# Performance work log

Hardware: AMD Instinct MI355X
Metric: run time of the kernel (lower is better)

The kernel has to match this reference:

```python
import jax, jax.numpy as jnp
import numpy as np

H = 16
D_MODEL = 1024
D_K = D_MODEL // H
WINDOW = 50
ROPE_BASE = 10000.0


def _rope_tables(seq_len, dim, dtype):
    inv_freq = 1.0 / (ROPE_BASE ** (jnp.arange(0, dim, 2, dtype=jnp.float32) / dim))
    t = jnp.arange(seq_len, dtype=jnp.float32)
    freqs = t[:, None] * inv_freq[None, :]          # [S, dim/2]
    emb = jnp.concatenate([freqs, freqs], axis=-1)  # [S, dim]
    return jnp.cos(emb).astype(dtype), jnp.sin(emb).astype(dtype)


def _rotate_half(x):
    d = x.shape[-1] // 2
    return jnp.concatenate([-x[..., d:], x[..., :d]], axis=-1)


def setup_inputs() -> dict:
    key = jax.random.key(0)
    ks = jax.random.split(key, 11)
    B, S = 2, 2048
    scale = 1.0 / np.sqrt(D_MODEL)
    inp = {
        'query': jax.random.normal(ks[0], (B, S, D_MODEL), jnp.float32),
        'key':   jax.random.normal(ks[1], (B, S, D_MODEL), jnp.float32),
        'value': jax.random.normal(ks[2], (B, S, D_MODEL), jnp.float32),
        'Wq': jax.random.normal(ks[3], (D_MODEL, D_MODEL), jnp.float32) * scale,
        'bq': jnp.zeros((D_MODEL,), jnp.float32),
        'Wk': jax.random.normal(ks[4], (D_MODEL, D_MODEL), jnp.float32) * scale,
        'bk': jnp.zeros((D_MODEL,), jnp.float32),
        'Wv': jax.random.normal(ks[5], (D_MODEL, D_MODEL), jnp.float32) * scale,
        'bv': jnp.zeros((D_MODEL,), jnp.float32),
        'Wo': jax.random.normal(ks[6], (D_MODEL, D_MODEL), jnp.float32) * scale,
        'bo': jnp.zeros((D_MODEL,), jnp.float32),
    }
    return inp


def reference(query, key, value, Wq, bq, Wk, bk, Wv, bv, Wo, bo):
    B, S, _ = query.shape
    # QKV projections (torch Linear: x @ W.T + b), split into heads -> [B,H,S,Dk]
    def proj(x, W, b):
        return (x @ W.T + b).reshape(B, S, H, D_K).transpose(0, 2, 1, 3)
    q = proj(query, Wq, bq)
    k = proj(key, Wk, bk)
    v = proj(value, Wv, bv)

    cos, sin = _rope_tables(S, D_K, q.dtype)  # [S, Dk]
    q = q * cos + _rotate_half(q) * sin
    k = k * cos + _rotate_half(k) * sin

    scores = jnp.einsum('bhqd,bhkd->bhqk', q, k) / np.sqrt(D_K)
    # sliding-window mask: |i-j| <= WINDOW
    idx = jnp.arange(S)
    dist = jnp.abs(idx[None, :] - idx[:, None])  # [S, S]
    scores = jnp.where(dist <= WINDOW, scores, jnp.asarray(-1e9, scores.dtype))

    p = jax.nn.softmax(scores, axis=-1)
    out = jnp.einsum('bhqk,bhkd->bhqd', p, v)          # [B,H,S,Dk]
    out = out.transpose(0, 2, 1, 3).reshape(B, S, D_MODEL)
    return out @ Wo.T + bo
```

## Files before the change

### kernel.cpp

```cpp
#include <hip/hip_runtime.h>
#include <hip/hip_bf16.h>
#include <math.h>

typedef __bf16 bf16_t;
typedef __bf16 bf16x8 __attribute__((ext_vector_type(8)));
typedef float floatx4 __attribute__((ext_vector_type(4)));
typedef unsigned int u32;
typedef unsigned short u16;

#define NHEAD 16

__device__ __forceinline__ void gload_lds16(const void* g, void* l) {
    __builtin_amdgcn_global_load_lds((const __attribute__((address_space(1))) u32*)g,
                                     (__attribute__((address_space(3))) u32*)l, 16, 0, 0);
}

__global__ __launch_bounds__(256) void k_prep(
    const float* __restrict__ q, const float* __restrict__ k, const float* __restrict__ v,
    const float* __restrict__ wq, const float* __restrict__ wk,
    const float* __restrict__ wv, const float* __restrict__ wo,
    bf16_t* __restrict__ Xq, bf16_t* __restrict__ Xk, bf16_t* __restrict__ Xv,
    bf16_t* __restrict__ Wqb, bf16_t* __restrict__ Wkb, bf16_t* __restrict__ Wvb,
    bf16_t* __restrict__ Wob, float* __restrict__ ct, float* __restrict__ st)
{
    int b = blockIdx.x;
    if (b < 8192) {
        const float* src; bf16_t* dst; int off;
        if      (b < 2048) { src = q;  dst = Xq;  off = b; }
        else if (b < 4096) { src = k;  dst = Xk;  off = b - 2048; }
        else if (b < 6144) { src = v;  dst = Xv;  off = b - 4096; }
        else if (b < 6656) { src = wq; dst = Wqb; off = b - 6144; }
        else if (b < 7168) { src = wk; dst = Wkb; off = b - 6656; }
        else if (b < 7680) { src = wv; dst = Wvb; off = b - 7168; }
        else               { src = wo; dst = Wob; off = b - 7680; }
        int i = (off * 256 + threadIdx.x) * 8;
        float4 a = *(const float4*)(src + i);
        float4 c = *(const float4*)(src + i + 4);
        bf16x8 o;
        o[0]=(bf16_t)a.x; o[1]=(bf16_t)a.y; o[2]=(bf16_t)a.z; o[3]=(bf16_t)a.w;
        o[4]=(bf16_t)c.x; o[5]=(bf16_t)c.y; o[6]=(bf16_t)c.z; o[7]=(bf16_t)c.w;
        *(bf16x8*)(dst + i) = o;
    } else {
        int idx = (b - 8192) * 256 + threadIdx.x;
        int s = idx >> 5, i = idx & 31;
        float e = (float)(2 * i) / 64.0f;
        float invf = 1.0f / powf(10000.0f, e);
        float ang = (float)s * invf;
        ct[idx] = cosf(ang);
        st[idx] = sinf(ang);
    }
}

__global__ __launch_bounds__(256,3) void k_gemm_qkv(
    const bf16_t* __restrict__ Xq, const bf16_t* __restrict__ Xk, const bf16_t* __restrict__ Xv,
    const bf16_t* __restrict__ Wqb, const bf16_t* __restrict__ Wkb, const bf16_t* __restrict__ Wvb,
    const float* __restrict__ bq, const float* __restrict__ bk, const float* __restrict__ bv,
    bf16_t* __restrict__ Qr, bf16_t* __restrict__ Kr, bf16_t* __restrict__ Vh,
    const float* __restrict__ ct, const float* __restrict__ st)
{
    __shared__ __align__(16) bf16_t As[2][4096];
    __shared__ __align__(16) bf16_t Bs[2][4096];

    int b0 = blockIdx.x;
    int wg = (b0 & 7) * 96 + (b0 >> 3);
    int id  = wg >> 8;
    int bid = wg & 255;

    const bf16_t* A   = (id==0) ? Xq  : (id==1) ? Xk  : Xv;
    const bf16_t* Wt  = (id==0) ? Wqb : (id==1) ? Wkb : Wvb;
    const float*  bias= (id==0) ? bq  : (id==1) ? bk  : bv;
    bf16_t* out = (id==0) ? Qr : (id==1) ? Kr : Vh;
    bool do_rope = (id < 2);

    int bm = (bid >> 3) << 7;
    int bn = (bid & 7) << 7;
    int tid = threadIdx.x;
    int l = tid & 63, wid = tid >> 6;
    int wr = wid >> 1, wc = wid & 1;
    int fr = l & 15, kg = l >> 4;

    floatx4 acc[4][4];
    #pragma unroll
    for (int i = 0; i < 4; ++i)
        #pragma unroll
        for (int j = 0; j < 4; ++j) acc[i][j] = (floatx4){0.f,0.f,0.f,0.f};

    int srow = tid >> 2;
    int scol = ((tid & 3) ^ (srow & 3)) << 3;
    const bf16_t* Ap0 = A  + ((size_t)(bm + srow) << 10) + scol;
    const bf16_t* Ap1 = A  + ((size_t)(bm + 64 + srow) << 10) + scol;
    const bf16_t* Bp0 = Wt + ((size_t)(bn + srow) << 10) + scol;
    const bf16_t* Bp1 = Wt + ((size_t)(bn + 64 + srow) << 10) + scol;

    gload_lds16(Ap0, &As[0][tid << 3]);
    gload_lds16(Ap1, &As[0][(tid + 256) << 3]);
    gload_lds16(Bp0, &Bs[0][tid << 3]);
    gload_lds16(Bp1, &Bs[0][(tid + 256) << 3]);
    __syncthreads();

    int a_off = fr * 64 + ((kg ^ (fr & 3)) << 4);
    int cur = 0;
    for (int t = 0; t < 32; ++t) {
        if (t < 31) {
            int k0 = (t + 1) << 5;
            gload_lds16(Ap0 + k0, &As[cur ^ 1][tid << 3]);
            gload_lds16(Ap1 + k0, &As[cur ^ 1][(tid + 256) << 3]);
            gload_lds16(Bp0 + k0, &Bs[cur ^ 1][tid << 3]);
            gload_lds16(Bp1 + k0, &Bs[cur ^ 1][(tid + 256) << 3]);
        }
        bf16x8 af[4], bfr[4];
        #pragma unroll
        for (int i = 0; i < 4; ++i)
            af[i]  = *(const bf16x8*)((const char*)As[cur] + (((wr << 2) + i) << 10) + a_off);
        #pragma unroll
        for (int j = 0; j < 4; ++j)
            bfr[j] = *(const bf16x8*)((const char*)Bs[cur] + (((wc << 2) + j) << 10) + a_off);
        #pragma unroll
        for (int i = 0; i < 4; ++i)
            #pragma unroll
            for (int j = 0; j < 4; ++j)
                acc[i][j] = __builtin_amdgcn_mfma_f32_16x16x32_bf16(af[i], bfr[j], acc[i][j], 0, 0, 0);
        __syncthreads();
        cur ^= 1;
    }

    int h = (bn + (wc<<6)) >> 6;
    #pragma unroll
    for (int i = 0; i < 4; ++i) {
        #pragma unroll
        for (int r = 0; r < 4; ++r) {
            int m  = bm + (wr<<6) + (i<<4) + (kg<<2) + r;
            int b_ = m >> 11, s_ = m & 2047;
            size_t ob = ((((size_t)(b_*NHEAD + h)) << 11) + s_) << 6;
            if (do_rope) {
                #pragma unroll
                for (int j = 0; j < 2; ++j) {
                    int d = (j<<4) + fr;
                    float lo = acc[i][j][r]   + bias[bn + (wc<<6) + d];
                    float hv = acc[i][j+2][r] + bias[bn + (wc<<6) + d + 32];
                    float c = ct[(s_<<5) + d], sn = st[(s_<<5) + d];
                    out[ob + d]      = (bf16_t)(lo*c - hv*sn);
                    out[ob + d + 32] = (bf16_t)(hv*c + lo*sn);
                }
            } else {
                #pragma unroll
                for (int j = 0; j < 4; ++j) {
                    int d = (j<<4) + fr;
                    out[ob + d] = (bf16_t)(acc[i][j][r] + bias[bn + (wc<<6) + d]);
                }
            }
        }
    }
}

__global__ __launch_bounds__(256,4) void k_gemm_o(
    const bf16_t* __restrict__ A, const bf16_t* __restrict__ Wt,
    const float* __restrict__ bias, float* __restrict__ out)
{
    __shared__ __align__(16) bf16_t As[2][2048];
    __shared__ __align__(16) bf16_t Bs[2][2048];

    int b0 = blockIdx.x;
    int wg = (b0 & 7) * 128 + (b0 >> 3);
    int bm = (wg >> 4) << 6;
    int bn = (wg & 15) << 6;
    int tid = threadIdx.x;
    int l = tid & 63, wid = tid >> 6;
    int fr = l & 15, kg = l >> 4;

    floatx4 acc[4];
    #pragma unroll
    for (int j = 0; j < 4; ++j) acc[j] = (floatx4){0.f,0.f,0.f,0.f};

    int srow = tid >> 2;
    int scol = ((tid & 3) ^ (srow & 3)) << 3;
    const bf16_t* Ap = A  + ((size_t)(bm + srow) << 10) + scol;
    const bf16_t* Bp = Wt + ((size_t)(bn + srow) << 10) + scol;

    gload_lds16(Ap, &As[0][tid << 3]);
    gload_lds16(Bp, &Bs[0][tid << 3]);
    __syncthreads();

    int a_off = fr * 64 + ((kg ^ (fr & 3)) << 4);
    int cur = 0;
    for (int t = 0; t < 32; ++t) {
        if (t < 31) {
            int k0 = (t + 1) << 5;
            gload_lds16(Ap + k0, &As[cur ^ 1][tid << 3]);
            gload_lds16(Bp + k0, &Bs[cur ^ 1][tid << 3]);
        }
        bf16x8 af, bfr[4];
        af = *(const bf16x8*)((const char*)As[cur] + (wid << 10) + a_off);
        #pragma unroll
        for (int j = 0; j < 4; ++j)
            bfr[j] = *(const bf16x8*)((const char*)Bs[cur] + (j << 10) + a_off);
        #pragma unroll
        for (int j = 0; j < 4; ++j)
            acc[j] = __builtin_amdgcn_mfma_f32_16x16x32_bf16(af, bfr[j], acc[j], 0, 0, 0);
        __syncthreads();
        cur ^= 1;
    }

    #pragma unroll
    for (int r = 0; r < 4; ++r) {
        int m = bm + (wid << 4) + (kg << 2) + r;
        #pragma unroll
        for (int j = 0; j < 4; ++j) {
            int n = bn + (j << 4) + fr;
            out[((size_t)m << 10) + n] = acc[j][r] + bias[n];
        }
    }
}

__global__ __launch_bounds__(256,3) void k_attn(
    const bf16_t* __restrict__ Qr, const bf16_t* __restrict__ Kr,
    const bf16_t* __restrict__ Vh, bf16_t* __restrict__ AO)
{
    __shared__ char smem[51200];
    char* KsPs = smem;
    char* VtB  = smem + 25600;

    int q0 = blockIdx.x << 6;
    int h = blockIdx.y, b_ = blockIdx.z;
    int kstart = q0 - 64; if (kstart < 0) kstart = 0;
    int kend   = q0 + 128; if (kend > 2048) kend = 2048;
    int NR = kend - kstart;

    int tid = threadIdx.x, l = tid & 63, w = tid >> 6;
    int lane16 = l & 15, hi8 = (l >> 4) << 3;

    const bf16_t* Kbase = Kr + (((((size_t)(b_*NHEAD + h)) << 11) + kstart) << 6);
    const bf16_t* Vbase = Vh + (((((size_t)(b_*NHEAD + h)) << 11) + kstart) << 6);

    #pragma unroll
    for (int it = 0; it < 6; ++it) {
        int c = tid + (it << 8);
        int y = c << 4;
        int row = y >> 7, oz = y & 127;
        int srw = row < NR ? row : NR - 1;
        int src = (srw << 7) + (oz ^ ((row & 7) << 4));
        gload_lds16((const char*)Kbase + src, KsPs + y);
    }
    #pragma unroll
    for (int it = 0; it < 6; ++it) {
        int c = tid + (it << 8);
        int jd2 = c >> 4;
        int dq  = (c & 15) << 2;
        int j0 = jd2 << 1, j1 = j0 + 1;
        int j0c = j0 < NR ? j0 : NR - 1;
        int j1c = j1 < NR ? j1 : NR - 1;
        ushort4 v0 = *(const ushort4*)(Vbase + (j0c << 6) + dq);
        ushort4 v1 = *(const ushort4*)(Vbase + (j1c << 6) + dq);
        u16 a0[4] = {(u16)v0.x,(u16)v0.y,(u16)v0.z,(u16)v0.w};
        u16 a1[4] = {(u16)v1.x,(u16)v1.y,(u16)v1.z,(u16)v1.w};
        #pragma unroll
        for (int t = 0; t < 4; ++t) {
            int d = dq + t;
            u32 pair = (u32)a0[t] | ((u32)a1[t] << 16);
            *(u32*)(VtB + d * 400 + ((jd2 << 2) ^ (((d >> 3) & 7) << 4))) = pair;
        }
    }
    int qs = q0 + (w << 4) + lane16;
    const bf16_t* Qbase = Qr + (((((size_t)(b_*NHEAD + h)) << 11) + qs) << 6);
    bf16x8 qf0 = *(const bf16x8*)(Qbase + hi8);
    bf16x8 qf1 = *(const bf16x8*)(Qbase + 32 + hi8);

    __syncthreads();

    floatx4 sc[12];
    #pragma unroll
    for (int kt = 0; kt < 12; ++kt) {
        int row = (kt << 4) + lane16;
        int base = (row << 7) + (hi8 << 1);
        int swz = (row & 7) << 4;
        bf16x8 kf0 = *(const bf16x8*)(KsPs + (base ^ swz));
        bf16x8 kf1 = *(const bf16x8*)(KsPs + ((base + 64) ^ swz));
        floatx4 a = (floatx4){0.f,0.f,0.f,0.f};
        a = __builtin_amdgcn_mfma_f32_16x16x32_bf16(qf0, kf0, a, 0, 0, 0);
        a = __builtin_amdgcn_mfma_f32_16x16x32_bf16(qf1, kf1, a, 0, 0, 0);
        sc[kt] = a;
    }

    float inv_[4];
    #pragma unroll
    for (int r = 0; r < 4; ++r) {
        int qrow = q0 + (w << 4) + ((l >> 4) << 2) + r;
        float mx = -1e30f;
        #pragma unroll
        for (int kt = 0; kt < 12; ++kt) {
            int ks = kstart + (kt << 4) + lane16;
            int dd = qrow - ks; dd = dd < 0 ? -dd : dd;
            float sv = sc[kt][r] * 0.125f;
            sv = (dd <= 50 && ks < kend) ? sv : -1e30f;
            sc[kt][r] = sv;
            mx = fmaxf(mx, sv);
        }
        #pragma unroll
        for (int off = 1; off < 16; off <<= 1) mx = fmaxf(mx, __shfl_xor(mx, off));
        float sum = 0.f;
        #pragma unroll
        for (int kt = 0; kt < 12; ++kt) {
            float p = __expf(sc[kt][r] - mx);
            sc[kt][r] = p;
            sum += p;
        }
        #pragma unroll
        for (int off = 1; off < 16; off <<= 1) sum += __shfl_xor(sum, off);
        inv_[r] = 1.0f / sum;
    }

    __syncthreads();

    char* PwB = KsPs + w * 6400;
    #pragma unroll
    for (int r = 0; r < 4; ++r) {
        int prow = ((l >> 4) << 2) + r;
        int pm = ((prow >> 2) & 3) << 4;
        #pragma unroll
        for (int kt = 0; kt < 12; ++kt) {
            int keyoff = ((kt << 4) + lane16) << 1;
            *(bf16_t*)(PwB + prow * 400 + (keyoff ^ pm)) = (bf16_t)(sc[kt][r] * inv_[r]);
        }
    }

    floatx4 oc[4];
    #pragma unroll
    for (int dt = 0; dt < 4; ++dt) oc[dt] = (floatx4){0.f,0.f,0.f,0.f};
    int pm_r = ((lane16 >> 2) & 3) << 4;
    #pragma unroll
    for (int ks = 0; ks < 6; ++ks) {
        int keyoff = ((ks << 5) + hi8) << 1;
        bf16x8 pf = *(const bf16x8*)(PwB + lane16 * 400 + (keyoff ^ pm_r));
        #pragma unroll
        for (int dt = 0; dt < 4; ++dt) {
            int d = (dt << 4) + lane16;
            bf16x8 vf = *(const bf16x8*)(VtB + d * 400 + (keyoff ^ (((d >> 3) & 7) << 4)));
            oc[dt] = __builtin_amdgcn_mfma_f32_16x16x32_bf16(pf, vf, oc[dt], 0, 0, 0);
        }
    }
    #pragma unroll
    for (int dt = 0; dt < 4; ++dt)
        #pragma unroll
        for (int r = 0; r < 4; ++r) {
            int qq = q0 + (w << 4) + ((l >> 4) << 2) + r;
            AO[(((size_t)(b_ * 2048 + qq)) << 10) + (h << 6) + (dt << 4) + lane16] = (bf16_t)oc[dt][r];
        }
}

extern "C" void kernel_launch(void* const* d_in, const int* in_sizes, int n_in,
                              void* d_out, int out_size, void* d_ws, size_t ws_size,
                              hipStream_t stream)
{
    const float* query = (const float*)d_in[0];
    const float* key_  = (const float*)d_in[1];
    const float* value = (const float*)d_in[2];
    const float* Wq = (const float*)d_in[3];
    const float* bq = (const float*)d_in[4];
    const float* Wk = (const float*)d_in[5];
    const float* bk = (const float*)d_in[6];
    const float* Wv = (const float*)d_in[7];
    const float* bv = (const float*)d_in[8];
    const float* Wo = (const float*)d_in[9];
    const float* bo = (const float*)d_in[10];

    char* ws = (char*)d_ws;
    bf16_t* Xq  = (bf16_t*)(ws);
    bf16_t* Xk  = (bf16_t*)(ws + 8388608);
    bf16_t* Xv  = (bf16_t*)(ws + 16777216);
    bf16_t* Wqb = (bf16_t*)(ws + 25165824);
    bf16_t* Wkb = (bf16_t*)(ws + 27262976);
    bf16_t* Wvb = (bf16_t*)(ws + 29360128);
    bf16_t* Wob = (bf16_t*)(ws + 31457280);
    bf16_t* Qr  = (bf16_t*)(ws + 33554432);
    bf16_t* Kr  = (bf16_t*)(ws + 41943040);
    bf16_t* Vh  = (bf16_t*)(ws + 50331648);
    bf16_t* AO  = (bf16_t*)(ws + 58720256);
    float*  ct  = (float*)(ws + 67108864);
    float*  st  = (float*)(ws + 67371008);

    k_prep<<<8448, 256, 0, stream>>>(query, key_, value, Wq, Wk, Wv, Wo,
                                     Xq, Xk, Xv, Wqb, Wkb, Wvb, Wob, ct, st);
    k_gemm_qkv<<<768, 256, 0, stream>>>(Xq, Xk, Xv, Wqb, Wkb, Wvb,
                                        bq, bk, bv, Qr, Kr, Vh, ct, st);
    k_attn<<<dim3(32, 16, 2), 256, 0, stream>>>(Qr, Kr, Vh, AO);
    k_gemm_o<<<1024, 256, 0, stream>>>(AO, Wob, bo, (float*)d_out);
}
```

Before: 94.12 us.

## Transpose attention MFMA operands, read K from global, vectorize P and output stores

The sliding-window attention kernel now reads K fragments straight from global memory instead of staging them in LDS, and swaps the MFMA operand order so each lane owns one query row. That makes the softmax reductions two cross-group shuffles instead of four-step reductions per row. P is written to LDS as packed 64-bit chunks, and the output is staged through LDS so global stores are coalesced 16-byte writes. It also adds s_setprio around the MFMA loops. The risk is uncoalesced, repeated global K reads that replace the shared LDS copy.

```diff
diff --git a/kernel.cpp b/kernel.cpp
--- a/kernel.cpp
+++ b/kernel.cpp
@@ -7,12 +7,18 @@
 typedef float floatx4 __attribute__((ext_vector_type(4)));
 typedef unsigned int u32;
 typedef unsigned short u16;
+typedef unsigned long long u64;
 
 #define NHEAD 16
 
 __device__ __forceinline__ void gload_lds16(const void* g, void* l) {
     __builtin_amdgcn_global_load_lds((const __attribute__((address_space(1))) u32*)g,
                                      (__attribute__((address_space(3))) u32*)l, 16, 0, 0);
+}
+
+__device__ __forceinline__ u32 pack2(float x, float y) {
+    bf16_t a = (bf16_t)x, b = (bf16_t)y;
+    return (u32)*(u16*)&a | ((u32)*(u16*)&b << 16);
 }
 
 __global__ __launch_bounds__(256) void k_prep(
@@ -217,8 +223,8 @@
     const bf16_t* __restrict__ Vh, bf16_t* __restrict__ AO)
 {
     __shared__ char smem[51200];
-    char* KsPs = smem;
-    char* VtB  = smem + 25600;
+    char* VtB  = smem;
+    char* Pall = smem + 25600;
 
     int q0 = blockIdx.x << 6;
     int h = blockIdx.y, b_ = blockIdx.z;
@@ -227,20 +233,11 @@
     int NR = kend - kstart;
 
     int tid = threadIdx.x, l = tid & 63, w = tid >> 6;
-    int lane16 = l & 15, hi8 = (l >> 4) << 3;
+    int q16 = l & 15, g = l >> 4, hi8 = g << 3;
 
     const bf16_t* Kbase = Kr + (((((size_t)(b_*NHEAD + h)) << 11) + kstart) << 6);
     const bf16_t* Vbase = Vh + (((((size_t)(b_*NHEAD + h)) << 11) + kstart) << 6);
 
-    #pragma unroll
-    for (int it = 0; it < 6; ++it) {
-        int c = tid + (it << 8);
-        int y = c << 4;
-        int row = y >> 7, oz = y & 127;
-        int srw = row < NR ? row : NR - 1;
-        int src = (srw << 7) + (oz ^ ((row & 7) << 4));
-        gload_lds16((const char*)Kbase + src, KsPs + y);
-    }
     #pragma unroll
     for (int it = 0; it < 6; ++it) {
         int c = tid + (it << 8);
@@ -260,91 +257,102 @@
             *(u32*)(VtB + d * 400 + ((jd2 << 2) ^ (((d >> 3) & 7) << 4))) = pair;
         }
     }
-    int qs = q0 + (w << 4) + lane16;
+
+    int qs = q0 + (w << 4) + q16;
     const bf16_t* Qbase = Qr + (((((size_t)(b_*NHEAD + h)) << 11) + qs) << 6);
     bf16x8 qf0 = *(const bf16x8*)(Qbase + hi8);
     bf16x8 qf1 = *(const bf16x8*)(Qbase + 32 + hi8);
 
-    __syncthreads();
-
     floatx4 sc[12];
+    __builtin_amdgcn_s_setprio(1);
     #pragma unroll
     for (int kt = 0; kt < 12; ++kt) {
-        int row = (kt << 4) + lane16;
-        int base = (row << 7) + (hi8 << 1);
-        int swz = (row & 7) << 4;
-        bf16x8 kf0 = *(const bf16x8*)(KsPs + (base ^ swz));
-        bf16x8 kf1 = *(const bf16x8*)(KsPs + ((base + 64) ^ swz));
+        int krow = (kt << 4) + q16;
+        int krc = krow < NR ? krow : NR - 1;
+        bf16x8 kf0 = *(const bf16x8*)(Kbase + (krc << 6) + hi8);
+        bf16x8 kf1 = *(const bf16x8*)(Kbase + (krc << 6) + 32 + hi8);
         floatx4 a = (floatx4){0.f,0.f,0.f,0.f};
-        a = __builtin_amdgcn_mfma_f32_16x16x32_bf16(qf0, kf0, a, 0, 0, 0);
-        a = __builtin_amdgcn_mfma_f32_16x16x32_bf16(qf1, kf1, a, 0, 0, 0);
+        a = __builtin_amdgcn_mfma_f32_16x16x32_bf16(kf0, qf0, a, 0, 0, 0);
+        a = __builtin_amdgcn_mfma_f32_16x16x32_bf16(kf1, qf1, a, 0, 0, 0);
         sc[kt] = a;
     }
-
-    float inv_[4];
-    #pragma unroll
-    for (int r = 0; r < 4; ++r) {
-        int qrow = q0 + (w << 4) + ((l >> 4) << 2) + r;
-        float mx = -1e30f;
-        #pragma unroll
-        for (int kt = 0; kt < 12; ++kt) {
-            int ks = kstart + (kt << 4) + lane16;
-            int dd = qrow - ks; dd = dd < 0 ? -dd : dd;
+    __builtin_amdgcn_s_setprio(0);
+
+    int qrow = q0 + (w << 4) + q16;
+    float mx = -1e30f;
+    #pragma unroll
+    for (int kt = 0; kt < 12; ++kt)
+        #pragma unroll
+        for (int r = 0; r < 4; ++r) {
+            int key = kstart + (kt << 4) + (g << 2) + r;
+            int dd = qrow - key; dd = dd < 0 ? -dd : dd;
             float sv = sc[kt][r] * 0.125f;
-            sv = (dd <= 50 && ks < kend) ? sv : -1e30f;
+            sv = (dd <= 50 && key < kend) ? sv : -1e30f;
             sc[kt][r] = sv;
             mx = fmaxf(mx, sv);
         }
-        #pragma unroll
-        for (int off = 1; off < 16; off <<= 1) mx = fmaxf(mx, __shfl_xor(mx, off));
-        float sum = 0.f;
-        #pragma unroll
-        for (int kt = 0; kt < 12; ++kt) {
+    mx = fmaxf(mx, __shfl_xor(mx, 16));
+    mx = fmaxf(mx, __shfl_xor(mx, 32));
+    float sum = 0.f;
+    #pragma unroll
+    for (int kt = 0; kt < 12; ++kt)
+        #pragma unroll
+        for (int r = 0; r < 4; ++r) {
             float p = __expf(sc[kt][r] - mx);
             sc[kt][r] = p;
             sum += p;
         }
-        #pragma unroll
-        for (int off = 1; off < 16; off <<= 1) sum += __shfl_xor(sum, off);
-        inv_[r] = 1.0f / sum;
+    sum += __shfl_xor(sum, 16);
+    sum += __shfl_xor(sum, 32);
+    float inv = 1.0f / sum;
+
+    char* PwB = Pall + w * 6400;
+    int swz = (q16 & 7) << 4;
+    #pragma unroll
+    for (int t = 0; t < 12; ++t) {
+        u32 lo = pack2(sc[t][0] * inv, sc[t][1] * inv);
+        u32 hi = pack2(sc[t][2] * inv, sc[t][3] * inv);
+        *(u64*)(PwB + q16 * 400 + (((t << 5) + (g << 3)) ^ swz)) = (u64)lo | ((u64)hi << 32);
     }
 
     __syncthreads();
 
-    char* PwB = KsPs + w * 6400;
-    #pragma unroll
-    for (int r = 0; r < 4; ++r) {
-        int prow = ((l >> 4) << 2) + r;
-        int pm = ((prow >> 2) & 3) << 4;
-        #pragma unroll
-        for (int kt = 0; kt < 12; ++kt) {
-            int keyoff = ((kt << 4) + lane16) << 1;
-            *(bf16_t*)(PwB + prow * 400 + (keyoff ^ pm)) = (bf16_t)(sc[kt][r] * inv_[r]);
-        }
-    }
-
     floatx4 oc[4];
     #pragma unroll
     for (int dt = 0; dt < 4; ++dt) oc[dt] = (floatx4){0.f,0.f,0.f,0.f};
-    int pm_r = ((lane16 >> 2) & 3) << 4;
-    #pragma unroll
-    for (int ks = 0; ks < 6; ++ks) {
-        int keyoff = ((ks << 5) + hi8) << 1;
-        bf16x8 pf = *(const bf16x8*)(PwB + lane16 * 400 + (keyoff ^ pm_r));
+    __builtin_amdgcn_s_setprio(1);
+    #pragma unroll
+    for (int kc = 0; kc < 6; ++kc) {
+        int keyoff = (kc << 6) + (g << 4);
+        bf16x8 pf = *(const bf16x8*)(PwB + q16 * 400 + (keyoff ^ swz));
         #pragma unroll
         for (int dt = 0; dt < 4; ++dt) {
-            int d = (dt << 4) + lane16;
+            int d = (dt << 4) + q16;
             bf16x8 vf = *(const bf16x8*)(VtB + d * 400 + (keyoff ^ (((d >> 3) & 7) << 4)));
-            oc[dt] = __builtin_amdgcn_mfma_f32_16x16x32_bf16(pf, vf, oc[dt], 0, 0, 0);
-        }
-    }
+            oc[dt] = __builtin_amdgcn_mfma_f32_16x16x32_bf16(vf, pf, oc[dt], 0, 0, 0);
+        }
+    }
+    __builtin_amdgcn_s_setprio(0);
+
+    asm volatile("s_waitcnt lgkmcnt(0)" ::: "memory");
+    __builtin_amdgcn_sched_barrier(0);
     #pragma unroll
     for (int dt = 0; dt < 4; ++dt)
         #pragma unroll
         for (int r = 0; r < 4; ++r) {
-            int qq = q0 + (w << 4) + ((l >> 4) << 2) + r;
-            AO[(((size_t)(b_ * 2048 + qq)) << 10) + (h << 6) + (dt << 4) + lane16] = (bf16_t)oc[dt][r];
-        }
+            int d = (dt << 4) + (g << 2) + r;
+            *(bf16_t*)(PwB + q16 * 400 + (d << 1)) = (bf16_t)oc[dt][r];
+        }
+    asm volatile("s_waitcnt lgkmcnt(0)" ::: "memory");
+    __builtin_amdgcn_sched_barrier(0);
+    #pragma unroll
+    for (int it = 0; it < 2; ++it) {
+        int c = l + (it << 6);
+        int row = c >> 3, off = (c & 7) << 4;
+        bf16x8 ov = *(const bf16x8*)(PwB + row * 400 + off);
+        int q_abs = q0 + (w << 4) + row;
+        *(bf16x8*)(AO + (((size_t)(b_ * 2048 + q_abs)) << 10) + (h << 6) + ((c & 7) << 3)) = ov;
+    }
 }
 
 extern "C" void kernel_launch(void* const* d_in, const int* in_sizes, int n_in,
```

Measured after the change: 103.1 us. 9.5% more time.
